# Performance work log

Hardware: AMD Instinct MI355X
Metric: run time of the kernel (lower is better)

Reference implementation:

```python
import jax, jax.numpy as jnp
import numpy as np

B, T, C, H, D, S = 4096, 256, 64, 16, 16, 10


def setup_inputs() -> dict:
    key = jax.random.key(0)
    ks = jax.random.split(key, 8)
    return {
        'states_seq': jax.random.uniform(ks[0], (B, T, S), dtype=jnp.float32) + 0.5,
        'covariates_seq': jax.random.normal(ks[1], (B, T, C), dtype=jnp.float32),
        'ln_gamma': jnp.ones((C,), jnp.float32),
        'ln_beta': jnp.zeros((C,), jnp.float32),
        'rnn_wx': jax.random.normal(ks[2], (C, H), dtype=jnp.float32) * 0.1,
        'rnn_wh': jax.random.normal(ks[3], (H, H), dtype=jnp.float32) * 0.1,
        'rnn_b': jnp.zeros((H,), jnp.float32),
        'd1_w': jax.random.normal(ks[4], (H, H), dtype=jnp.float32) * 0.1,
        'd1_b': jnp.zeros((H,), jnp.float32),
        'd2_w': jax.random.normal(ks[5], (H, D), dtype=jnp.float32) * 0.1,
        'd2_b': jnp.zeros((D,), jnp.float32),
    }


def _cash_budget(s, d):
    # Deterministic cash-budget accounting update.
    # s: (B, 10) = [rev_prev, cash, AR, inventory, PPE, AP, debt, equity, retained, other]
    # d: (B, 16) drivers; first 10 used as ratios.
    sig = jax.nn.sigmoid
    g      = jnp.tanh(d[:, 0]) * 0.2      # sales growth
    cogs_m = sig(d[:, 1])                 # COGS margin
    opex_m = sig(d[:, 2]) * 0.5           # opex margin
    dep_r  = sig(d[:, 3]) * 0.1           # depreciation rate on PPE
    capex_r = sig(d[:, 4]) * 0.2          # capex as % of revenue
    dso = sig(d[:, 5])                    # AR ratio
    dio = sig(d[:, 6])                    # inventory ratio
    dpo = sig(d[:, 7])                    # AP ratio
    tax_r = sig(d[:, 8]) * 0.35           # tax rate
    int_r = sig(d[:, 9]) * 0.1            # interest rate on debt

    rev_prev, cash, ar, inv, ppe, ap, debt, equity, re, other = [s[:, i] for i in range(10)]
    rev = rev_prev * (1.0 + g)
    cogs = cogs_m * rev
    opex = opex_m * rev
    dep = dep_r * ppe
    interest = int_r * debt
    ebt = rev - cogs - opex - dep - interest
    tax = tax_r * jnp.maximum(ebt, 0.0)
    ni = ebt - tax
    ar_new = dso * rev
    inv_new = dio * cogs
    ap_new = dpo * cogs
    capex = capex_r * rev
    ppe_new = ppe + capex - dep
    cash_new = cash + ni + dep - capex - (ar_new - ar) - (inv_new - inv) + (ap_new - ap)
    re_new = re + ni
    s_next = jnp.stack([rev, cash_new, ar_new, inv_new, ppe_new, ap_new, debt, equity, re_new, other], axis=-1)
    is_out = jnp.stack([rev, cogs, opex, dep, interest, tax, ni], axis=-1)  # (B, 7)
    return s_next, is_out


def reference(states_seq, covariates_seq, ln_gamma, ln_beta, rnn_wx, rnn_wh, rnn_b, d1_w, d1_b, d2_w, d2_b):
    # LayerNormalization (keras default eps=1e-3, last axis)
    mu = covariates_seq.mean(-1, keepdims=True)
    var = covariates_seq.var(-1, keepdims=True)
    x = (covariates_seq - mu) * jax.lax.rsqrt(var + 1e-3) * ln_gamma + ln_beta

    # SimpleRNN: h_t = tanh(x_t Wx + h_{t-1} Wh + b), return_sequences
    xw = jnp.einsum('btc,ch->bth', x, rnn_wx) + rnn_b  # precompute input projection

    def rnn_step(h, xt):
        h = jnp.tanh(xt + h @ rnn_wh)
        return h, h

    h0 = jnp.zeros((x.shape[0], rnn_wh.shape[0]), x.dtype)
    _, hs = jax.lax.scan(rnn_step, h0, jnp.swapaxes(xw, 0, 1))  # (T, B, H)
    hs = jnp.swapaxes(hs, 0, 1)  # (B, T, H)

    drivers = jnp.tanh(hs @ d1_w + d1_b) @ d2_w + d2_b  # (B, T, D)

    # Cash-budget recurrence over t = 1 .. T-1
    def cb_step(s_prev, d_t):
        s_next, is_out = _cash_budget(s_prev, d_t)
        return s_next, (s_next, is_out)

    s0 = states_seq[:, 0, :]
    _, (states_tm, is_tm) = jax.lax.scan(cb_step, s0, jnp.swapaxes(drivers[:, 1:, :], 0, 1))
    states_pred = jnp.swapaxes(states_tm, 0, 1)  # (B, T-1, 10)
    is_pred = jnp.swapaxes(is_tm, 0, 1)          # (B, T-1, 7)
    return states_pred, is_pred
```

## Files before the change

### kernel.cpp

```cpp
#include <hip/hip_runtime.h>
#include <hip/hip_fp16.h>

#define NB 4096
#define NT 256
#define NC 64
#define NH 16
#define NS 10
#define NTO 255

__device__ __forceinline__ float fast_rcp(float x){ return __builtin_amdgcn_rcpf(x); }
__device__ __forceinline__ float fast_rsq(float x){ return __builtin_amdgcn_rsqf(x); }
__device__ __forceinline__ float fsig(float x){ return fast_rcp(1.0f + __expf(-x)); }
__device__ __forceinline__ float ftanh(float x){
    float e = __expf(2.0f*x);
    return fmaf(-2.0f, fast_rcp(e + 1.0f), 1.0f);
}

template<int R>
__device__ __forceinline__ float rotf(float x){
    return __int_as_float(__builtin_amdgcn_update_dpp(
        0, __float_as_int(x), 0x120 + R, 0xF, 0xF, true));
}
__device__ __forceinline__ float row_bcast_sum(float x){
    x += rotf<8>(x);
    x += rotf<4>(x);
    x += rotf<2>(x);
    x += rotf<1>(x);
    return x;
}
__device__ __forceinline__ float rotdot16_4(float v, const float* w, float acc){
    float a1 = 0.f, a2 = 0.f, a3 = 0.f;
    acc = fmaf(v,           w[0],  acc);
    a1  = fmaf(rotf<1>(v),  w[1],  a1);
    a2  = fmaf(rotf<2>(v),  w[2],  a2);
    a3  = fmaf(rotf<3>(v),  w[3],  a3);
    acc = fmaf(rotf<4>(v),  w[4],  acc);
    a1  = fmaf(rotf<5>(v),  w[5],  a1);
    a2  = fmaf(rotf<6>(v),  w[6],  a2);
    a3  = fmaf(rotf<7>(v),  w[7],  a3);
    acc = fmaf(rotf<8>(v),  w[8],  acc);
    a1  = fmaf(rotf<9>(v),  w[9],  a1);
    a2  = fmaf(rotf<10>(v), w[10], a2);
    a3  = fmaf(rotf<11>(v), w[11], a3);
    acc = fmaf(rotf<12>(v), w[12], acc);
    a1  = fmaf(rotf<13>(v), w[13], a1);
    a2  = fmaf(rotf<14>(v), w[14], a2);
    a3  = fmaf(rotf<15>(v), w[15], a3);
    return (acc + a1) + (a2 + a3);
}

__global__ __launch_bounds__(256, 4) void xw_kernel(
    const float* __restrict__ cov, const float* __restrict__ lng,
    const float* __restrict__ lnb, const float* __restrict__ wx,
    const float* __restrict__ rnb, __half* __restrict__ xws)
{
    const int wid  = threadIdx.x >> 6;
    const int lane = threadIdx.x & 63;
    const int g = lane >> 4, l = lane & 15;
    const int b = (blockIdx.x << 2) + wid;

    float gwr[64];
    #pragma unroll
    for (int r = 0; r < 16; ++r) {
        int c0 = 4 * ((l - r) & 15);
        #pragma unroll
        for (int j = 0; j < 4; ++j)
            gwr[4*r+j] = lng[c0+j] * wx[(c0+j)*NH + l];
    }
    float bwb = rnb[l];
    #pragma unroll
    for (int c = 0; c < NC; ++c) bwb = fmaf(lnb[c], wx[c*NH + l], bwb);

    const float4* gp = (const float4*)cov + (size_t)b*NT*16 + g*16 + l;
    __half* op = xws + ((size_t)b*16 + l)*NT + g;

    float4 cur = gp[0];
    float4 nxt = gp[64];
    #pragma unroll 2
    for (int it = 0; it < 64; ++it) {
        float4 x = cur;
        cur = nxt;
        if (it < 62) nxt = gp[(size_t)(it+2)*64];
        float ss = (x.x + x.y) + (x.z + x.w);
        float sq = fmaf(x.x,x.x, fmaf(x.y,x.y, fmaf(x.z,x.z, x.w*x.w)));
        ss = row_bcast_sum(ss);
        sq = row_bcast_sum(sq);
        float mu  = ss * (1.0f/64.0f);
        float var = fmaf(-mu, mu, sq * (1.0f/64.0f));
        float rs  = fast_rsq(var + 0.001f);
        float nmu = -mu * rs;
        float x0 = fmaf(x.x, rs, nmu), x1 = fmaf(x.y, rs, nmu);
        float x2 = fmaf(x.z, rs, nmu), x3 = fmaf(x.w, rs, nmu);
        float a0 = bwb, a1 = 0.f, a2 = 0.f, a3 = 0.f;
        a0 = fmaf(x0, gwr[0], a0); a1 = fmaf(x1, gwr[1], a1);
        a2 = fmaf(x2, gwr[2], a2); a3 = fmaf(x3, gwr[3], a3);
#define ROTSTEP(R) { float r0=rotf<R>(x0), r1=rotf<R>(x1), r2=rotf<R>(x2), r3=rotf<R>(x3); \
        a0=fmaf(r0,gwr[4*R+0],a0); a1=fmaf(r1,gwr[4*R+1],a1); \
        a2=fmaf(r2,gwr[4*R+2],a2); a3=fmaf(r3,gwr[4*R+3],a3); }
        ROTSTEP(1)  ROTSTEP(2)  ROTSTEP(3)  ROTSTEP(4)  ROTSTEP(5)
        ROTSTEP(6)  ROTSTEP(7)  ROTSTEP(8)  ROTSTEP(9)  ROTSTEP(10)
        ROTSTEP(11) ROTSTEP(12) ROTSTEP(13) ROTSTEP(14) ROTSTEP(15)
#undef ROTSTEP
        float xw = (a0+a1)+(a2+a3);
        op[it*4] = __float2half(xw);
    }
}

__global__ __launch_bounds__(64, 1) void scan_kernel(
    const float* __restrict__ states, const __half* __restrict__ xws,
    const float* __restrict__ wh,     const float* __restrict__ d1w,
    const float* __restrict__ d1b,    const float* __restrict__ d2w,
    const float* __restrict__ d2b,    float* __restrict__ out)
{
    const int lane = threadIdx.x;
    const int g = lane >> 4, l = lane & 15;
    const int b = (blockIdx.x << 2) + g;

    __shared__ __align__(16) float db[8*64];

    float whr[NH], d1r[NH], d2r[NH];
    #pragma unroll
    for (int r = 0; r < NH; ++r) {
        int src = (l - r) & 15;
        whr[r] = wh[src*NH + l];
        d1r[r] = d1w[src*NH + l];
        d2r[r] = d2w[src*NH + l];
    }
    const float d1bl = d1b[l], d2bl = d2b[l];
    const float Aa = (l==0)?0.4f:(l==2)?0.5f:(l==3)?0.1f:(l==4)?0.2f:(l==8)?0.35f:(l==9)?0.1f:1.0f;
    const float Ba = (l==0)?2.0f:1.0f;
    const float Ca = (l==0)?-0.2f:0.0f;

    float s0,s1,s2,s3,s4,s5,s6,s7,s8,s9;
    { const float* sp = states + (size_t)b*NT*NS;
      s0=sp[0];s1=sp[1];s2=sp[2];s3=sp[3];s4=sp[4];
      s5=sp[5];s6=sp[6];s7=sp[7];s8=sp[8];s9=sp[9]; }

    float* spo = out + (size_t)b*NTO*NS + l;
    float* ipo = out + (size_t)NB*NTO*NS + (size_t)b*NTO*7 + l;

    const ushort4* xp = (const ushort4*)(xws + ((size_t)b*16 + l)*NT);
    ushort4 xa = xp[0], xb = xp[1];

    float h = 0.f;

#define BSLOT(T) (((T)&7)<<6)

#define RNN(XWV)  h = ftanh(rotdot16_4(h, whr, (XWV)))

#define MLP(T) do { \
    float t1 = ftanh(rotdot16_4(h, d1r, d1bl)); \
    float dv = rotdot16_4(t1, d2r, d2bl); \
    db[BSLOT(T) + lane] = fmaf(Aa, fsig(Ba*dv), Ca); \
} while(0)

#define BUDGET(T) do { \
    const float* rb = db + BSLOT(T) + (g<<4); \
    float4 w0 = *(const float4*)rb; \
    float4 w1 = *(const float4*)(rb+4); \
    float2 w2 = *(const float2*)(rb+8); \
    float rev   = fmaf(s0, w0.x, s0); \
    float cogs  = w0.y * rev; \
    float opex  = w0.z * rev; \
    float dep   = w0.w * s4; \
    float inte  = w2.y * s6; \
    float ebt   = (((rev - cogs) - opex) - dep) - inte; \
    float tax   = w2.x * fmaxf(ebt, 0.0f); \
    float ni    = ebt - tax; \
    float arn   = w1.y * rev; \
    float invn  = w1.z * cogs; \
    float apn   = w1.w * cogs; \
    float capex = w1.x * rev; \
    float ppen  = (s4 + capex) - dep; \
    float cashn = (((((s1 + ni) + dep) - capex) - (arn - s2)) - (invn - s3)) + (apn - s5); \
    float ren   = s8 + ni; \
    s0=rev; s1=cashn; s2=arn; s3=invn; s4=ppen; s5=apn; s8=ren; \
    float sv = (l==0)?rev:(l==1)?cashn:(l==2)?arn:(l==3)?invn:(l==4)?ppen: \
               (l==5)?apn:(l==6)?s6:(l==7)?s7:(l==8)?ren:s9; \
    float iv = (l==0)?rev:(l==1)?cogs:(l==2)?opex:(l==3)?dep:(l==4)?inte:(l==5)?tax:ni; \
    if (l < NS) *spo = sv; \
    if (l < 7)  *ipo = iv; \
    spo += NS; ipo += 7; \
} while(0)

#define XH(V,U) __half2float(__ushort_as_half((U)==0?(V).x:(U)==1?(V).y:(U)==2?(V).z:(V).w))

    {
        ushort4 xc = xa; xa = xb; xb = xp[2];
        RNN(XH(xc,0));
        RNN(XH(xc,1)); MLP(1);
        RNN(XH(xc,2)); BUDGET(1); MLP(2);
        RNN(XH(xc,3)); BUDGET(2); MLP(3);
    }

    #pragma unroll 1
    for (int tt = 1; tt < 64; ++tt) {
        ushort4 xc = xa; xa = xb;
        if (tt < 62) xb = xp[tt+2];
        #pragma unroll
        for (int u = 0; u < 4; ++u) {
            const int t = tt*4 + u;
            RNN(XH(xc,u));
            BUDGET(t-1);
            MLP(t);
        }
    }

    BUDGET(255);

#undef XH
#undef BUDGET
#undef MLP
#undef RNN
#undef BSLOT
}

extern "C" void kernel_launch(void* const* d_in, const int* in_sizes, int n_in,
                              void* d_out, int out_size, void* d_ws, size_t ws_size,
                              hipStream_t stream) {
    (void)in_sizes; (void)n_in; (void)ws_size; (void)out_size;
    __half* xws = (__half*)d_ws;
    xw_kernel<<<NB/4, 256, 0, stream>>>(
        (const float*)d_in[1],
        (const float*)d_in[2],
        (const float*)d_in[3],
        (const float*)d_in[4],
        (const float*)d_in[6],
        xws);
    scan_kernel<<<NB/4, 64, 0, stream>>>(
        (const float*)d_in[0],
        xws,
        (const float*)d_in[5],
        (const float*)d_in[7],
        (const float*)d_in[8],
        (const float*)d_in[9],
        (const float*)d_in[10],
        (float*)d_out);
}
```

Baseline: 589.0 us.

## Software-pipeline RNN, MLP layers and budget across staggered timesteps

Restructures the scan kernel into a four-stage software pipeline. At each step the RNN update for step t, the first dense layer for t-1, the second dense layer for t-2 and the cash-budget update for t-3 are all interleaved. The RNN and first dense layer now share the same 15 DPP rotations of h. This gives more independent instruction-level parallelism per step and removes redundant cross-lane rotations, which matters for the latency-bound single-wave blocks. The cost is higher register pressure and extra prologue/epilogue steps.

New measurement: 583.5 us. About the same (-0.9%).

```diff
diff --git a/kernel.cpp b/kernel.cpp
--- a/kernel.cpp
+++ b/kernel.cpp
@@ -27,26 +27,6 @@
     x += rotf<2>(x);
     x += rotf<1>(x);
     return x;
-}
-__device__ __forceinline__ float rotdot16_4(float v, const float* w, float acc){
-    float a1 = 0.f, a2 = 0.f, a3 = 0.f;
-    acc = fmaf(v,           w[0],  acc);
-    a1  = fmaf(rotf<1>(v),  w[1],  a1);
-    a2  = fmaf(rotf<2>(v),  w[2],  a2);
-    a3  = fmaf(rotf<3>(v),  w[3],  a3);
-    acc = fmaf(rotf<4>(v),  w[4],  acc);
-    a1  = fmaf(rotf<5>(v),  w[5],  a1);
-    a2  = fmaf(rotf<6>(v),  w[6],  a2);
-    a3  = fmaf(rotf<7>(v),  w[7],  a3);
-    acc = fmaf(rotf<8>(v),  w[8],  acc);
-    a1  = fmaf(rotf<9>(v),  w[9],  a1);
-    a2  = fmaf(rotf<10>(v), w[10], a2);
-    a3  = fmaf(rotf<11>(v), w[11], a3);
-    acc = fmaf(rotf<12>(v), w[12], acc);
-    a1  = fmaf(rotf<13>(v), w[13], a1);
-    a2  = fmaf(rotf<14>(v), w[14], a2);
-    a3  = fmaf(rotf<15>(v), w[15], a3);
-    return (acc + a1) + (a2 + a3);
 }
 
 __global__ __launch_bounds__(256, 4) void xw_kernel(
@@ -143,76 +123,122 @@
     ushort4 xa = xp[0], xb = xp[1];
 
     float h = 0.f;
-
-#define BSLOT(T) (((T)&7)<<6)
-
-#define RNN(XWV)  h = ftanh(rotdot16_4(h, whr, (XWV)))
-
-#define MLP(T) do { \
-    float t1 = ftanh(rotdot16_4(h, d1r, d1bl)); \
-    float dv = rotdot16_4(t1, d2r, d2bl); \
-    db[BSLOT(T) + lane] = fmaf(Aa, fsig(Ba*dv), Ca); \
+    float t1p = 0.f;
+
+#define XH(V,U) __half2float(__ushort_as_half((U)==0?(V).x:(U)==1?(V).y:(U)==2?(V).z:(V).w))
+
+#define STEP(J, XWV, S1F, S2F, S3F, S4F) do { \
+     \
+    float4 w0{}, w1{}; float2 w2{}; \
+    if (S4F) { const float* rb = db + ((((J)-3)&7)<<6) + (g<<4); \
+        w0 = *(const float4*)rb; w1 = *(const float4*)(rb+4); w2 = *(const float2*)(rb+8); } \
+    float hn = h, t1n = t1p; \
+    float eR = 0.f, eD = 0.f, sR = 0.f, sD = 0.f; \
+    if (S1F || S2F) { \
+        float r1=rotf<1>(h),  r2=rotf<2>(h),  r3=rotf<3>(h),  r4=rotf<4>(h); \
+        float r5=rotf<5>(h),  r6=rotf<6>(h),  r7=rotf<7>(h),  r8=rotf<8>(h); \
+        float r9=rotf<9>(h),  r10=rotf<10>(h), r11=rotf<11>(h), r12=rotf<12>(h); \
+        float r13=rotf<13>(h), r14=rotf<14>(h), r15=rotf<15>(h); \
+        float aR0=(XWV), aR1=0.f, aR2=0.f, aR3=0.f; \
+        float aD0=d1bl,  aD1=0.f, aD2=0.f, aD3=0.f; \
+        if (S1F) aR0=fmaf(h,  whr[0], aR0);   if (S2F) aD0=fmaf(h,  d1r[0], aD0); \
+        if (S1F) aR1=fmaf(r1, whr[1], aR1);   if (S2F) aD1=fmaf(r1, d1r[1], aD1); \
+        if (S1F) aR2=fmaf(r2, whr[2], aR2);   if (S2F) aD2=fmaf(r2, d1r[2], aD2); \
+        if (S1F) aR3=fmaf(r3, whr[3], aR3);   if (S2F) aD3=fmaf(r3, d1r[3], aD3); \
+        if (S1F) aR0=fmaf(r4, whr[4], aR0);   if (S2F) aD0=fmaf(r4, d1r[4], aD0); \
+        if (S1F) aR1=fmaf(r5, whr[5], aR1);   if (S2F) aD1=fmaf(r5, d1r[5], aD1); \
+        if (S1F) aR2=fmaf(r6, whr[6], aR2);   if (S2F) aD2=fmaf(r6, d1r[6], aD2); \
+        if (S1F) aR3=fmaf(r7, whr[7], aR3);   if (S2F) aD3=fmaf(r7, d1r[7], aD3); \
+        if (S1F) aR0=fmaf(r8, whr[8], aR0);   if (S2F) aD0=fmaf(r8, d1r[8], aD0); \
+        if (S1F) aR1=fmaf(r9, whr[9], aR1);   if (S2F) aD1=fmaf(r9, d1r[9], aD1); \
+        if (S1F) aR2=fmaf(r10,whr[10],aR2);   if (S2F) aD2=fmaf(r10,d1r[10],aD2); \
+        if (S1F) aR3=fmaf(r11,whr[11],aR3);   if (S2F) aD3=fmaf(r11,d1r[11],aD3); \
+        if (S1F) aR0=fmaf(r12,whr[12],aR0);   if (S2F) aD0=fmaf(r12,d1r[12],aD0); \
+        if (S1F) aR1=fmaf(r13,whr[13],aR1);   if (S2F) aD1=fmaf(r13,d1r[13],aD1); \
+        if (S1F) aR2=fmaf(r14,whr[14],aR2);   if (S2F) aD2=fmaf(r14,d1r[14],aD2); \
+        if (S1F) aR3=fmaf(r15,whr[15],aR3);   if (S2F) aD3=fmaf(r15,d1r[15],aD3); \
+        if (S1F) sR = (aR0+aR1)+(aR2+aR3); \
+        if (S2F) sD = (aD0+aD1)+(aD2+aD3); \
+        if (S1F) eR = __expf(2.0f*sR); \
+        if (S2F) eD = __expf(2.0f*sD); \
+    } \
+     \
+    float dv = 0.f; \
+    if (S3F) { \
+        float q1=rotf<1>(t1p),  q2=rotf<2>(t1p),  q3=rotf<3>(t1p),  q4=rotf<4>(t1p); \
+        float q5=rotf<5>(t1p),  q6=rotf<6>(t1p),  q7=rotf<7>(t1p),  q8=rotf<8>(t1p); \
+        float q9=rotf<9>(t1p),  q10=rotf<10>(t1p), q11=rotf<11>(t1p), q12=rotf<12>(t1p); \
+        float q13=rotf<13>(t1p), q14=rotf<14>(t1p), q15=rotf<15>(t1p); \
+        float aS0=d2bl, aS1=0.f, aS2=0.f, aS3=0.f; \
+        aS0=fmaf(t1p,d2r[0],aS0); aS1=fmaf(q1, d2r[1], aS1); \
+        aS2=fmaf(q2, d2r[2], aS2); aS3=fmaf(q3, d2r[3], aS3); \
+        aS0=fmaf(q4, d2r[4], aS0); aS1=fmaf(q5, d2r[5], aS1); \
+        aS2=fmaf(q6, d2r[6], aS2); aS3=fmaf(q7, d2r[7], aS3); \
+        aS0=fmaf(q8, d2r[8], aS0); aS1=fmaf(q9, d2r[9], aS1); \
+        aS2=fmaf(q10,d2r[10],aS2); aS3=fmaf(q11,d2r[11],aS3); \
+        aS0=fmaf(q12,d2r[12],aS0); aS1=fmaf(q13,d2r[13],aS1); \
+        aS2=fmaf(q14,d2r[14],aS2); aS3=fmaf(q15,d2r[15],aS3); \
+        dv = (aS0+aS1)+(aS2+aS3); \
+    } \
+     \
+    if (S1F) hn  = fmaf(-2.0f, fast_rcp(eR+1.0f), 1.0f); \
+    if (S2F) t1n = fmaf(-2.0f, fast_rcp(eD+1.0f), 1.0f); \
+    if (S3F) { \
+        float es = __expf(-Ba*dv); \
+        float act = fmaf(Aa, fast_rcp(1.0f+es), Ca); \
+        db[((((J)-2)&7)<<6) + lane] = act; \
+    } \
+    if (S4F) { \
+        float rev   = fmaf(s0, w0.x, s0); \
+        float cogs  = w0.y * rev; \
+        float opex  = w0.z * rev; \
+        float dep   = w0.w * s4; \
+        float inte  = w2.y * s6; \
+        float ebt   = (((rev - cogs) - opex) - dep) - inte; \
+        float tax   = w2.x * fmaxf(ebt, 0.0f); \
+        float ni    = ebt - tax; \
+        float arn   = w1.y * rev; \
+        float invn  = w1.z * cogs; \
+        float apn   = w1.w * cogs; \
+        float capex = w1.x * rev; \
+        float ppen  = (s4 + capex) - dep; \
+        float cashn = (((((s1 + ni) + dep) - capex) - (arn - s2)) - (invn - s3)) + (apn - s5); \
+        float ren   = s8 + ni; \
+        s0=rev; s1=cashn; s2=arn; s3=invn; s4=ppen; s5=apn; s8=ren; \
+        float sv = (l==0)?rev:(l==1)?cashn:(l==2)?arn:(l==3)?invn:(l==4)?ppen: \
+                   (l==5)?apn:(l==6)?s6:(l==7)?s7:(l==8)?ren:s9; \
+        float iv = (l==0)?rev:(l==1)?cogs:(l==2)?opex:(l==3)?dep:(l==4)?inte:(l==5)?tax:ni; \
+        if (l < NS) *spo = sv; \
+        if (l < 7)  *ipo = iv; \
+        spo += NS; ipo += 7; \
+    } \
+    h = hn; t1p = t1n; \
 } while(0)
-
-#define BUDGET(T) do { \
-    const float* rb = db + BSLOT(T) + (g<<4); \
-    float4 w0 = *(const float4*)rb; \
-    float4 w1 = *(const float4*)(rb+4); \
-    float2 w2 = *(const float2*)(rb+8); \
-    float rev   = fmaf(s0, w0.x, s0); \
-    float cogs  = w0.y * rev; \
-    float opex  = w0.z * rev; \
-    float dep   = w0.w * s4; \
-    float inte  = w2.y * s6; \
-    float ebt   = (((rev - cogs) - opex) - dep) - inte; \
-    float tax   = w2.x * fmaxf(ebt, 0.0f); \
-    float ni    = ebt - tax; \
-    float arn   = w1.y * rev; \
-    float invn  = w1.z * cogs; \
-    float apn   = w1.w * cogs; \
-    float capex = w1.x * rev; \
-    float ppen  = (s4 + capex) - dep; \
-    float cashn = (((((s1 + ni) + dep) - capex) - (arn - s2)) - (invn - s3)) + (apn - s5); \
-    float ren   = s8 + ni; \
-    s0=rev; s1=cashn; s2=arn; s3=invn; s4=ppen; s5=apn; s8=ren; \
-    float sv = (l==0)?rev:(l==1)?cashn:(l==2)?arn:(l==3)?invn:(l==4)?ppen: \
-               (l==5)?apn:(l==6)?s6:(l==7)?s7:(l==8)?ren:s9; \
-    float iv = (l==0)?rev:(l==1)?cogs:(l==2)?opex:(l==3)?dep:(l==4)?inte:(l==5)?tax:ni; \
-    if (l < NS) *spo = sv; \
-    if (l < 7)  *ipo = iv; \
-    spo += NS; ipo += 7; \
-} while(0)
-
-#define XH(V,U) __half2float(__ushort_as_half((U)==0?(V).x:(U)==1?(V).y:(U)==2?(V).z:(V).w))
 
     {
         ushort4 xc = xa; xa = xb; xb = xp[2];
-        RNN(XH(xc,0));
-        RNN(XH(xc,1)); MLP(1);
-        RNN(XH(xc,2)); BUDGET(1); MLP(2);
-        RNN(XH(xc,3)); BUDGET(2); MLP(3);
+        h = ftanh(XH(xc,0));
+        STEP(1, XH(xc,1), 1,0,0,0);
+        STEP(2, XH(xc,2), 1,1,0,0);
+        STEP(3, XH(xc,3), 1,1,1,0);
     }
 
     #pragma unroll 1
     for (int tt = 1; tt < 64; ++tt) {
         ushort4 xc = xa; xa = xb;
         if (tt < 62) xb = xp[tt+2];
-        #pragma unroll
-        for (int u = 0; u < 4; ++u) {
-            const int t = tt*4 + u;
-            RNN(XH(xc,u));
-            BUDGET(t-1);
-            MLP(t);
-        }
-    }
-
-    BUDGET(255);
-
+        STEP(4*tt+0, XH(xc,0), 1,1,1,1);
+        STEP(4*tt+1, XH(xc,1), 1,1,1,1);
+        STEP(4*tt+2, XH(xc,2), 1,1,1,1);
+        STEP(4*tt+3, XH(xc,3), 1,1,1,1);
+    }
+
+    STEP(256, 0.0f, 0,1,1,1);
+    STEP(257, 0.0f, 0,0,1,1);
+    STEP(258, 0.0f, 0,0,0,1);
+
+#undef STEP
 #undef XH
-#undef BUDGET
-#undef MLP
-#undef RNN
-#undef BSLOT
 }
 
 extern "C" void kernel_launch(void* const* d_in, const int* in_sizes, int n_in,
```
